# Performance work log

Hardware: AMD Instinct MI355X
Metric: run time of the kernel (lower is better)

The kernel has to match this reference:

```python
import jax, jax.numpy as jnp
import numpy as np

N_NODES = 100000


def _gcn_norm(edge_index, edge_weight, num_nodes):
    # add self loops with weight 1 (PyG GCNConv default)
    loop = jnp.arange(num_nodes, dtype=edge_index.dtype)
    src = jnp.concatenate([edge_index[0], loop])
    dst = jnp.concatenate([edge_index[1], loop])
    w = jnp.concatenate([edge_weight, jnp.ones(num_nodes, edge_weight.dtype)])
    deg = jax.ops.segment_sum(w, dst, num_segments=num_nodes)
    dinv = jnp.where(deg > 0, jax.lax.rsqrt(deg), 0.0).astype(edge_weight.dtype)
    norm = dinv[src] * w * dinv[dst]
    return src, dst, norm


def _gcn_conv(x, W, b, src, dst, norm):
    h = x @ W                                   # [N, out]
    msg = h[src] * norm[:, None]                # [E+N, out] gather + scale
    out = jax.ops.segment_sum(msg, dst, num_segments=x.shape[0])
    return out + b


def setup_inputs() -> dict:
    key = jax.random.key(0)
    ks = jax.random.split(key, 6)
    nfeat, nhid, nclass, E = 128, 64, 40, 1600000
    return {
        "x": jax.random.normal(ks[0], (N_NODES, nfeat), jnp.float32),
        "edge_index": jax.random.randint(ks[1], (2, E), 0, N_NODES, jnp.int64),
        "edge_weight": jax.random.uniform(ks[2], (E,), jnp.float32),
        "W1": jax.random.normal(ks[3], (nfeat, nhid), jnp.float32) / np.sqrt(nfeat),
        "b1": jnp.zeros((nhid,), jnp.float32),
        "W2": jax.random.normal(ks[4], (nhid, nclass), jnp.float32) / np.sqrt(nhid),
        "b2": jnp.zeros((nclass,), jnp.float32),
    }


def reference(x, edge_index, edge_weight, W1, b1, W2, b2):
    src, dst, norm = _gcn_norm(edge_index, edge_weight, x.shape[0])
    h = jax.nn.relu(_gcn_conv(x, W1, b1, src, dst, norm))
    # dropout p=0.0 / eval mode -> identity
    h = _gcn_conv(h, W2, b2, src, dst, norm)
    return jax.nn.log_softmax(h, axis=1)
```

## Files before the change

### kernel.cpp

```cpp
#include <hip/hip_runtime.h>
#include <hip/hip_fp16.h>
#include <math.h>

#define NFEAT 128
#define NHID 64
#define NCLASS 40
#define BNODES 256
#define BSHIFT 8
#define EPB 4096
#define CAPSH 13
#define CAP (1 << CAPSH)
#define LCAP 5120

typedef _Float16 f16x8 __attribute__((ext_vector_type(8)));
typedef float f32x4 __attribute__((ext_vector_type(4)));

static __device__ __forceinline__ __half2 i2h2(int x) { union { int i; __half2 h; } u; u.i = x; return u.h; }
static __device__ __forceinline__ int h22i(__half2 h) { union { int i; __half2 h; } u; u.h = h; return u.i; }
static __device__ __forceinline__ __half2 shfl_xor_h2(__half2 v, int off) { return i2h2(__shfl_xor(h22i(v), off)); }


__global__ void k_init(int* __restrict__ gcur, int NB) {
    int i = blockIdx.x * blockDim.x + threadIdx.x;
    if (i < NB) gcur[i] = i << CAPSH;
}

__global__ __launch_bounds__(256) void k_bscatter(const int* __restrict__ src, const int* __restrict__ dst,
                                                  const float* __restrict__ w, int* __restrict__ gcur,
                                                  int2* __restrict__ csrT, int E, int NB) {
    __shared__ int2 sorted[EPB];
    __shared__ int gidx[EPB];
    __shared__ int lcnt[512], lscan[512], fb[512], lpos[512];
    int t = threadIdx.x;
    for (int i = t; i < 512; i += 256) { lcnt[i] = 0; lpos[i] = 0; }
    __syncthreads();
    int base = blockIdx.x * EPB;
    int rs[16], rd[16]; float rw[16];
    #pragma unroll
    for (int j = 0; j < 4; j++) {
        int e0 = base + j * 1024 + t * 4;
        if (e0 + 3 < E) {
            int4 s4 = *(const int4*)(src + e0);
            int4 d4 = *(const int4*)(dst + e0);
            float4 w4 = *(const float4*)(w + e0);
            rs[j * 4 + 0] = s4.x; rs[j * 4 + 1] = s4.y; rs[j * 4 + 2] = s4.z; rs[j * 4 + 3] = s4.w;
            rd[j * 4 + 0] = d4.x; rd[j * 4 + 1] = d4.y; rd[j * 4 + 2] = d4.z; rd[j * 4 + 3] = d4.w;
            rw[j * 4 + 0] = w4.x; rw[j * 4 + 1] = w4.y; rw[j * 4 + 2] = w4.z; rw[j * 4 + 3] = w4.w;
        } else {
            #pragma unroll
            for (int k = 0; k < 4; k++) {
                int e = e0 + k;
                bool ok = (e < E);
                rd[j * 4 + k] = ok ? dst[e] : -1;
                rs[j * 4 + k] = ok ? src[e] : 0;
                rw[j * 4 + k] = ok ? w[e] : 0.f;
            }
        }
    }
    #pragma unroll
    for (int i = 0; i < 16; i++)
        if (rd[i] >= 0) atomicAdd(&lcnt[rd[i] >> BSHIFT], 1);
    __syncthreads();
    int i0 = t, i1 = t + 256;
    lscan[i0] = lcnt[i0]; lscan[i1] = lcnt[i1];
    __syncthreads();
    for (int off = 1; off < 512; off <<= 1) {
        int v0 = (i0 >= off) ? lscan[i0 - off] : 0;
        int v1 = (i1 >= off) ? lscan[i1 - off] : 0;
        __syncthreads();
        lscan[i0] += v0; lscan[i1] += v1;
        __syncthreads();
    }
    for (int i = t; i < NB; i += 256) {
        int c = lcnt[i];
        if (c) {
            int gb = atomicAdd(&gcur[i], c);
            fb[i] = gb - (lscan[i] - c);
        }
    }
    __syncthreads();
    #pragma unroll
    for (int i = 0; i < 16; i++) {
        if (rd[i] >= 0) {
            int d = rd[i];
            int b = d >> BSHIFT;
            int p = (lscan[b] - lcnt[b]) + atomicAdd(&lpos[b], 1);
            int2 v;
            v.x = rs[i] | ((d & (BNODES - 1)) << 20);
            v.y = __float_as_int(rw[i]);
            sorted[p] = v;
            gidx[p] = fb[b] + p;
        }
    }
    __syncthreads();
    int tot = lscan[511];
    for (int i = t; i < tot; i += 256) csrT[gidx[i]] = sorted[i];
}

__global__ __launch_bounds__(512) void k_cscan(const int* __restrict__ gcur, int* __restrict__ cbase, int NB) {
    __shared__ int sh[512];
    int t = threadIdx.x;
    int c = (t < NB) ? (gcur[t] - (t << CAPSH)) : 0;
    sh[t] = c;
    __syncthreads();
    for (int off = 1; off < 512; off <<= 1) {
        int v = (t >= off) ? sh[t - off] : 0;
        __syncthreads();
        sh[t] += v;
        __syncthreads();
    }
    if (t < NB) cbase[t] = sh[t] - c;
}

__global__ __launch_bounds__(256) void k_lsort(const int* __restrict__ gcur, const int* __restrict__ cbase,
                                               const int2* __restrict__ csrT, int2* __restrict__ csr,
                                               int* __restrict__ offs, float* __restrict__ dinv,
                                               int N, int E) {
    __shared__ int2 sorted[LCAP];
    __shared__ int lh[BNODES];
    __shared__ int lo[BNODES];
    __shared__ float da[BNODES];
    int b = blockIdx.x, t = threadIdx.x;
    int rbase = b << CAPSH;
    int cnt = gcur[b] - rbase;
    if (cnt > LCAP) cnt = LCAP;
    int cb = cbase[b];
    lh[t] = 0; da[t] = 0.f;
    __syncthreads();
    int2 reg[20];
    #pragma unroll
    for (int i = 0; i < 20; i++) {
        int e = t + i * 256;
        reg[i] = (e < cnt) ? csrT[rbase + e] : make_int2(-1, 0);
    }
    #pragma unroll
    for (int i = 0; i < 20; i++) {
        if (reg[i].x >= 0) {
            int dl = (reg[i].x >> 20) & 255;
            atomicAdd(&lh[dl], 1);
            atomicAdd(&da[dl], __int_as_float(reg[i].y));
        }
    }
    __syncthreads();
    int own = lh[t];
    lo[t] = own;
    __syncthreads();
    for (int off = 1; off < 256; off <<= 1) {
        int v = (t >= off) ? lo[t - off] : 0;
        __syncthreads();
        lo[t] += v;
        __syncthreads();
    }
    int excl = lo[t] - own;
    __syncthreads();
    lh[t] = excl;
    int gn = (b << BSHIFT) + t;
    if (gn < N) {
        offs[gn] = cb + excl;
        dinv[gn] = rsqrtf(1.0f + da[t]);
    }
    if (b == 0 && t == 0) offs[N] = E;
    __syncthreads();
    #pragma unroll
    for (int i = 0; i < 20; i++) {
        if (reg[i].x >= 0) {
            int dl = (reg[i].x >> 20) & 255;
            int p = atomicAdd(&lh[dl], 1);
            sorted[p] = reg[i];
        }
    }
    __syncthreads();
    for (int e = t; e < cnt; e += 256) {
        int2 v = sorted[e];
        __half2 w2 = __half2half2(__float2half(__int_as_float(v.y)));
        v.x &= 0xFFFFF;
        v.y = h22i(w2);
        csr[cb + e] = v;
    }
}


__global__ __launch_bounds__(256) void k_gemm1(const float* __restrict__ x,
                                               const float* __restrict__ W,
                                               const float* __restrict__ dinv,
                                               __half* __restrict__ h, int N) {
    __shared__ _Float16 xh[64][136];
    __shared__ _Float16 Wt[64][136];
    int t = threadIdx.x;
    int row0 = blockIdx.x * 64;
    for (int i = t; i < 2048; i += 256) {
        int r = i >> 5, k4 = i & 31;
        int row = row0 + r;
        float4 v = (row < N) ? ((const float4*)(x + (size_t)row * NFEAT))[k4]
                             : make_float4(0.f, 0.f, 0.f, 0.f);
        *(__half2*)&xh[r][k4 * 4]     = __floats2half2_rn(v.x, v.y);
        *(__half2*)&xh[r][k4 * 4 + 2] = __floats2half2_rn(v.z, v.w);
    }
    for (int i = t; i < 4096; i += 256) {
        int k2 = i >> 6, c = i & 63;
        float a0 = W[(size_t)(2 * k2) * NHID + c];
        float a1 = W[(size_t)(2 * k2 + 1) * NHID + c];
        *(__half2*)&Wt[c][k2 * 2] = __floats2half2_rn(a0, a1);
    }
    __syncthreads();
    int wave = t >> 6, lane = t & 63;
    int quad = lane >> 4, l16 = lane & 15;
    int r0 = wave * 16;
    f32x4 acc[4] = {};
    #pragma unroll
    for (int k0 = 0; k0 < 128; k0 += 32) {
        f16x8 af = *(const f16x8*)&xh[r0 + l16][k0 + quad * 8];
        #pragma unroll
        for (int ct = 0; ct < 4; ct++) {
            f16x8 bf = *(const f16x8*)&Wt[ct * 16 + l16][k0 + quad * 8];
            acc[ct] = __builtin_amdgcn_mfma_f32_16x16x32_f16(af, bf, acc[ct], 0, 0, 0);
        }
    }
    #pragma unroll
    for (int ct = 0; ct < 4; ct++) {
        #pragma unroll
        for (int j = 0; j < 4; j++) {
            int row = row0 + r0 + quad * 4 + j;
            if (row < N)
                h[(size_t)row * NHID + ct * 16 + l16] = __float2half(dinv[row] * acc[ct][j]);
        }
    }
}


__global__ __launch_bounds__(256) void k_agg1(const int* __restrict__ offs, const int2* __restrict__ csr,
                                              const __half* __restrict__ h1, const float* __restrict__ dinv,
                                              const float* __restrict__ b1, __half* __restrict__ out1, int N) {
    int n = (blockIdx.x * blockDim.x + threadIdx.x) >> 6;
    if (n >= N) return;
    int lane = threadIdx.x & 63;
    int grp = lane >> 3;
    int c8 = lane & 7;
    const char* hb = (const char*)h1;
    unsigned int c16 = (unsigned int)c8 << 4;
    int e = offs[n], end = offs[n + 1];
    float di = dinv[n];
    float4 hsv = *(const float4*)(hb + (unsigned int)n * 128u + c16);
    float4 bb0 = ((const float4*)b1)[2 * c8];
    float4 bb1 = ((const float4*)b1)[2 * c8 + 1];
    __half2 z = __floats2half2_rn(0.f, 0.f);
    __half2 aA[4] = {z, z, z, z}, aB[4] = {z, z, z, z};
    for (; e + 16 <= end; e += 16) {
        int2 vA = csr[e + grp];
        int2 vB = csr[e + 8 + grp];
        float4 hA = *(const float4*)(hb + (unsigned int)(vA.x & 0xFFFFF) * 128u + c16);
        float4 hB = *(const float4*)(hb + (unsigned int)(vB.x & 0xFFFFF) * 128u + c16);
        __half2 wA = i2h2(vA.y), wB = i2h2(vB.y);
        const __half2* pA = (const __half2*)&hA;
        const __half2* pB = (const __half2*)&hB;
        #pragma unroll
        for (int q = 0; q < 4; q++) {
            aA[q] = __hfma2(wA, pA[q], aA[q]);
            aB[q] = __hfma2(wB, pB[q], aB[q]);
        }
    }
    if (e + 8 <= end) {
        int2 v = csr[e + grp];
        float4 hv = *(const float4*)(hb + (unsigned int)(v.x & 0xFFFFF) * 128u + c16);
        __half2 wv = i2h2(v.y);
        const __half2* p = (const __half2*)&hv;
        #pragma unroll
        for (int q = 0; q < 4; q++) aA[q] = __hfma2(wv, p[q], aA[q]);
        e += 8;
    }
    if (e + grp < end) {
        int2 v = csr[e + grp];
        float4 hv = *(const float4*)(hb + (unsigned int)(v.x & 0xFFFFF) * 128u + c16);
        __half2 wv = i2h2(v.y);
        const __half2* p = (const __half2*)&hv;
        #pragma unroll
        for (int q = 0; q < 4; q++) aB[q] = __hfma2(wv, p[q], aB[q]);
    }
    __half2 acc2[4];
    #pragma unroll
    for (int q = 0; q < 4; q++) acc2[q] = __hadd2(aA[q], aB[q]);
    #pragma unroll
    for (int off = 8; off <= 32; off <<= 1) {
        #pragma unroll
        for (int q = 0; q < 4; q++) acc2[q] = __hadd2(acc2[q], shfl_xor_h2(acc2[q], off));
    }
    if (grp == 0) {
        float a[8], s[8];
        #pragma unroll
        for (int q = 0; q < 4; q++) {
            float2 fa = __half22float2(acc2[q]);
            a[2 * q] = fa.x; a[2 * q + 1] = fa.y;
            float2 f = __half22float2(((const __half2*)&hsv)[q]);
            s[2 * q] = f.x; s[2 * q + 1] = f.y;
        }
        float o[8];
        o[0] = fmaxf(di * (a[0] + s[0]) + bb0.x, 0.f);
        o[1] = fmaxf(di * (a[1] + s[1]) + bb0.y, 0.f);
        o[2] = fmaxf(di * (a[2] + s[2]) + bb0.z, 0.f);
        o[3] = fmaxf(di * (a[3] + s[3]) + bb0.w, 0.f);
        o[4] = fmaxf(di * (a[4] + s[4]) + bb1.x, 0.f);
        o[5] = fmaxf(di * (a[5] + s[5]) + bb1.y, 0.f);
        o[6] = fmaxf(di * (a[6] + s[6]) + bb1.z, 0.f);
        o[7] = fmaxf(di * (a[7] + s[7]) + bb1.w, 0.f);
        float4 st;
        #pragma unroll
        for (int q = 0; q < 4; q++)
            ((__half2*)&st)[q] = __floats2half2_rn(o[2 * q], o[2 * q + 1]);
        ((float4*)out1)[(size_t)n * 8 + c8] = st;
    }
}


__global__ __launch_bounds__(256) void k_gemm2(const __half* __restrict__ a,
                                               const float* __restrict__ W,
                                               const float* __restrict__ dinv,
                                               __half* __restrict__ h, int N) {
    __shared__ _Float16 As[64][72];
    __shared__ _Float16 Bt[64][72];
    int t = threadIdx.x;
    int row0 = blockIdx.x * 64;
    for (int i = t; i < 512; i += 256) {
        int r = i >> 3, q = i & 7;
        int row = row0 + r;
        f16x8 v = {};
        if (row < N) v = *(const f16x8*)(a + (size_t)row * NHID + q * 8);
        *(f16x8*)&As[r][q * 8] = v;
    }
    for (int i = t; i < 4096; i += 256) {
        int c = i >> 6, k = i & 63;
        float wv = (c < NCLASS) ? W[k * NCLASS + c] : 0.f;
        Bt[c][k] = (_Float16)wv;
    }
    __syncthreads();
    int wave = t >> 6, lane = t & 63;
    int quad = lane >> 4, l16 = lane & 15;
    int r0 = wave * 16;
    f32x4 acc[4] = {};
    #pragma unroll
    for (int k0 = 0; k0 < 64; k0 += 32) {
        f16x8 af = *(const f16x8*)&As[r0 + l16][k0 + quad * 8];
        #pragma unroll
        for (int ct = 0; ct < 4; ct++) {
            f16x8 bf = *(const f16x8*)&Bt[ct * 16 + l16][k0 + quad * 8];
            acc[ct] = __builtin_amdgcn_mfma_f32_16x16x32_f16(af, bf, acc[ct], 0, 0, 0);
        }
    }
    #pragma unroll
    for (int ct = 0; ct < 4; ct++) {
        int col = ct * 16 + l16;
        #pragma unroll
        for (int j = 0; j < 4; j++) {
            int row = row0 + r0 + quad * 4 + j;
            if (row < N)
                h[((size_t)row << 6) + col] = __float2half(dinv[row] * acc[ct][j]);
        }
    }
}


__global__ __launch_bounds__(256) void k_agg2(const int* __restrict__ offs, const int2* __restrict__ csr,
                                              const __half* __restrict__ h2, const float* __restrict__ dinv,
                                              const float* __restrict__ b2, float* __restrict__ out, int N) {
    int n = (blockIdx.x * blockDim.x + threadIdx.x) >> 6;
    if (n >= N) return;
    int lane = threadIdx.x & 63;
    int grp = lane >> 3;
    int c8 = lane & 7;
    const char* hb = (const char*)h2;
    unsigned int c16 = (unsigned int)c8 << 4;
    int e = offs[n], end = offs[n + 1];
    bool act = (c8 < 5);
    float di = dinv[n];
    float4 hsv = *(const float4*)(hb + ((unsigned int)n << 7) + c16);
    float4 bb0 = {}, bb1 = {};
    if (act) {
        bb0 = ((const float4*)b2)[2 * c8];
        bb1 = ((const float4*)b2)[2 * c8 + 1];
    }
    __half2 z = __floats2half2_rn(0.f, 0.f);
    __half2 aA[4] = {z, z, z, z}, aB[4] = {z, z, z, z};
    for (; e + 16 <= end; e += 16) {
        int2 vA = csr[e + grp];
        int2 vB = csr[e + 8 + grp];
        float4 hA = *(const float4*)(hb + ((unsigned int)(vA.x & 0xFFFFF) << 7) + c16);
        float4 hB = *(const float4*)(hb + ((unsigned int)(vB.x & 0xFFFFF) << 7) + c16);
        __half2 wA = i2h2(vA.y), wB = i2h2(vB.y);
        const __half2* pA = (const __half2*)&hA;
        const __half2* pB = (const __half2*)&hB;
        #pragma unroll
        for (int q = 0; q < 4; q++) {
            aA[q] = __hfma2(wA, pA[q], aA[q]);
            aB[q] = __hfma2(wB, pB[q], aB[q]);
        }
    }
    if (e + 8 <= end) {
        int2 v = csr[e + grp];
        float4 hv = *(const float4*)(hb + ((unsigned int)(v.x & 0xFFFFF) << 7) + c16);
        __half2 wv = i2h2(v.y);
        const __half2* p = (const __half2*)&hv;
        #pragma unroll
        for (int q = 0; q < 4; q++) aA[q] = __hfma2(wv, p[q], aA[q]);
        e += 8;
    }
    if (e + grp < end) {
        int2 v = csr[e + grp];
        float4 hv = *(const float4*)(hb + ((unsigned int)(v.x & 0xFFFFF) << 7) + c16);
        __half2 wv = i2h2(v.y);
        const __half2* p = (const __half2*)&hv;
        #pragma unroll
        for (int q = 0; q < 4; q++) aB[q] = __hfma2(wv, p[q], aB[q]);
    }
    __half2 acc2[4];
    #pragma unroll
    for (int q = 0; q < 4; q++) acc2[q] = __hadd2(aA[q], aB[q]);
    #pragma unroll
    for (int off = 8; off <= 32; off <<= 1) {
        #pragma unroll
        for (int q = 0; q < 4; q++) acc2[q] = __hadd2(acc2[q], shfl_xor_h2(acc2[q], off));
    }
    float a[8], s[8];
    #pragma unroll
    for (int q = 0; q < 4; q++) {
        float2 fa = __half22float2(acc2[q]);
        a[2 * q] = fa.x; a[2 * q + 1] = fa.y;
        float2 f = __half22float2(((const __half2*)&hsv)[q]);
        s[2 * q] = f.x; s[2 * q + 1] = f.y;
    }
    float v[8];
    v[0] = di * (a[0] + s[0]) + bb0.x;
    v[1] = di * (a[1] + s[1]) + bb0.y;
    v[2] = di * (a[2] + s[2]) + bb0.z;
    v[3] = di * (a[3] + s[3]) + bb0.w;
    v[4] = di * (a[4] + s[4]) + bb1.x;
    v[5] = di * (a[5] + s[5]) + bb1.y;
    v[6] = di * (a[6] + s[6]) + bb1.z;
    v[7] = di * (a[7] + s[7]) + bb1.w;
    float m = -INFINITY;
    if (act) {
        #pragma unroll
        for (int k = 0; k < 8; k++) m = fmaxf(m, v[k]);
    }
    #pragma unroll
    for (int off = 1; off <= 4; off <<= 1) m = fmaxf(m, __shfl_xor(m, off));
    float ex = 0.f;
    if (act) {
        #pragma unroll
        for (int k = 0; k < 8; k++) ex += __expf(v[k] - m);
    }
    #pragma unroll
    for (int off = 1; off <= 4; off <<= 1) ex += __shfl_xor(ex, off);
    if (act && grp == 0) {
        float ls = __logf(ex);
        float4 o0, o1;
        o0.x = v[0] - m - ls; o0.y = v[1] - m - ls; o0.z = v[2] - m - ls; o0.w = v[3] - m - ls;
        o1.x = v[4] - m - ls; o1.y = v[5] - m - ls; o1.z = v[6] - m - ls; o1.w = v[7] - m - ls;
        float* op = out + (size_t)n * NCLASS + c8 * 8;
        *(float4*)op = o0;
        *(float4*)(op + 4) = o1;
    }
}


extern "C" void kernel_launch(void* const* d_in, const int* in_sizes, int n_in,
                              void* d_out, int out_size, void* d_ws, size_t ws_size,
                              hipStream_t stream) {
    const float* x  = (const float*)d_in[0];
    const int*   ei = (const int*)d_in[1];
    const float* w  = (const float*)d_in[2];
    const float* W1 = (const float*)d_in[3];
    const float* b1 = (const float*)d_in[4];
    const float* W2 = (const float*)d_in[5];
    const float* b2 = (const float*)d_in[6];
    float* out = (float*)d_out;

    const int N = in_sizes[0] / NFEAT;
    const int E = in_sizes[1] / 2;
    const int* src = ei;
    const int* dst = ei + E;

    const int NB = (N + BNODES - 1) >> BSHIFT;
    const int nbuild = (E + EPB - 1) / EPB;

    int2*   csrT  = (int2*)d_ws;
    int2*   csr   = csrT + (size_t)NB * CAP;
    float*  dinv  = (float*)(csr + E);
    int*    offs  = (int*)(dinv + N);
    __half* h1h   = (__half*)(offs + N + 1);
    __half* out1h = h1h + (size_t)N * NHID;
    __half* h2old = out1h + (size_t)N * NHID;
    int*    gcur  = (int*)(h2old + (size_t)N * NCLASS);
    int*    cbase = gcur + NB;

    __half* h2p = (__half*)d_ws;

    k_init<<<(NB + 255) / 256, 256, 0, stream>>>(gcur, NB);
    k_bscatter<<<nbuild, 256, 0, stream>>>(src, dst, w, gcur, csrT, E, NB);
    k_cscan<<<1, 512, 0, stream>>>(gcur, cbase, NB);
    k_lsort<<<NB, 256, 0, stream>>>(gcur, cbase, csrT, csr, offs, dinv, N, E);

    k_gemm1<<<(N + 63) / 64, 256, 0, stream>>>(x, W1, dinv, h1h, N);
    k_agg1<<<(N + 3) / 4, 256, 0, stream>>>(offs, csr, h1h, dinv, b1, out1h, N);

    k_gemm2<<<(N + 63) / 64, 256, 0, stream>>>(out1h, W2, dinv, h2p, N);
    k_agg2<<<(N + 3) / 4, 256, 0, stream>>>(offs, csr, h2p, dinv, b2, out, N);
}
```

Before: 275.9 us.

## Sort CSR in place per bucket, drop global scan, and prefetch four edge batches

The per-bucket local sort now writes back into the same padded bucket region instead of compacting into a separate CSR array. That removes the single-block prefix-scan kernel and one full copy of the edge array. Each node therefore stores an explicit end offset, since bucket regions are no longer contiguous. The aggregation kernels also issue four predicated edge gathers up front to raise memory-level parallelism, then fall back to a simple strided tail loop. The in-place read-then-write within a block relies on all loads finishing before the stores, which the existing barriers ensure, and the padded layout spreads CSR reads over more memory.

```diff
diff --git a/kernel.cpp b/kernel.cpp
--- a/kernel.cpp
+++ b/kernel.cpp
@@ -97,25 +97,10 @@
     for (int i = t; i < tot; i += 256) csrT[gidx[i]] = sorted[i];
 }
 
-__global__ __launch_bounds__(512) void k_cscan(const int* __restrict__ gcur, int* __restrict__ cbase, int NB) {
-    __shared__ int sh[512];
-    int t = threadIdx.x;
-    int c = (t < NB) ? (gcur[t] - (t << CAPSH)) : 0;
-    sh[t] = c;
-    __syncthreads();
-    for (int off = 1; off < 512; off <<= 1) {
-        int v = (t >= off) ? sh[t - off] : 0;
-        __syncthreads();
-        sh[t] += v;
-        __syncthreads();
-    }
-    if (t < NB) cbase[t] = sh[t] - c;
-}
-
-__global__ __launch_bounds__(256) void k_lsort(const int* __restrict__ gcur, const int* __restrict__ cbase,
-                                               const int2* __restrict__ csrT, int2* __restrict__ csr,
-                                               int* __restrict__ offs, float* __restrict__ dinv,
-                                               int N, int E) {
+__global__ __launch_bounds__(256) void k_lsort(const int* __restrict__ gcur,
+                                               int2* csr,
+                                               int* __restrict__ offs, int* __restrict__ endo,
+                                               float* __restrict__ dinv, int N) {
     __shared__ int2 sorted[LCAP];
     __shared__ int lh[BNODES];
     __shared__ int lo[BNODES];
@@ -124,14 +109,13 @@
     int rbase = b << CAPSH;
     int cnt = gcur[b] - rbase;
     if (cnt > LCAP) cnt = LCAP;
-    int cb = cbase[b];
     lh[t] = 0; da[t] = 0.f;
     __syncthreads();
     int2 reg[20];
     #pragma unroll
     for (int i = 0; i < 20; i++) {
         int e = t + i * 256;
-        reg[i] = (e < cnt) ? csrT[rbase + e] : make_int2(-1, 0);
+        reg[i] = (e < cnt) ? csr[rbase + e] : make_int2(-1, 0);
     }
     #pragma unroll
     for (int i = 0; i < 20; i++) {
@@ -156,10 +140,10 @@
     lh[t] = excl;
     int gn = (b << BSHIFT) + t;
     if (gn < N) {
-        offs[gn] = cb + excl;
+        offs[gn] = rbase + excl;
+        endo[gn] = rbase + excl + own;
         dinv[gn] = rsqrtf(1.0f + da[t]);
     }
-    if (b == 0 && t == 0) offs[N] = E;
     __syncthreads();
     #pragma unroll
     for (int i = 0; i < 20; i++) {
@@ -175,7 +159,7 @@
         __half2 w2 = __half2half2(__float2half(__int_as_float(v.y)));
         v.x &= 0xFFFFF;
         v.y = h22i(w2);
-        csr[cb + e] = v;
+        csr[rbase + e] = v;
     }
 }
 
@@ -228,7 +212,8 @@
 }
 
 
-__global__ __launch_bounds__(256) void k_agg1(const int* __restrict__ offs, const int2* __restrict__ csr,
+__global__ __launch_bounds__(256) void k_agg1(const int* __restrict__ offs, const int* __restrict__ endo,
+                                              const int2* __restrict__ csr,
                                               const __half* __restrict__ h1, const float* __restrict__ dinv,
                                               const float* __restrict__ b1, __half* __restrict__ out1, int N) {
     int n = (blockIdx.x * blockDim.x + threadIdx.x) >> 6;
@@ -238,47 +223,59 @@
     int c8 = lane & 7;
     const char* hb = (const char*)h1;
     unsigned int c16 = (unsigned int)c8 << 4;
-    int e = offs[n], end = offs[n + 1];
+    int e = offs[n], end = endo[n];
     float di = dinv[n];
     float4 hsv = *(const float4*)(hb + (unsigned int)n * 128u + c16);
     float4 bb0 = ((const float4*)b1)[2 * c8];
     float4 bb1 = ((const float4*)b1)[2 * c8 + 1];
     __half2 z = __floats2half2_rn(0.f, 0.f);
-    __half2 aA[4] = {z, z, z, z}, aB[4] = {z, z, z, z};
-    for (; e + 16 <= end; e += 16) {
-        int2 vA = csr[e + grp];
-        int2 vB = csr[e + 8 + grp];
-        float4 hA = *(const float4*)(hb + (unsigned int)(vA.x & 0xFFFFF) * 128u + c16);
-        float4 hB = *(const float4*)(hb + (unsigned int)(vB.x & 0xFFFFF) * 128u + c16);
-        __half2 wA = i2h2(vA.y), wB = i2h2(vB.y);
-        const __half2* pA = (const __half2*)&hA;
-        const __half2* pB = (const __half2*)&hB;
+    __half2 aa0[4] = {z, z, z, z}, aa1[4] = {z, z, z, z};
+    __half2 aa2[4] = {z, z, z, z}, aa3[4] = {z, z, z, z};
+    {
+        int2 v0, v1, v2, v3;
+        int i0 = e + grp, i1 = e + 8 + grp, i2 = e + 16 + grp, i3 = e + 24 + grp;
+        bool b0 = i0 < end, b1v = i1 < end, b2 = i2 < end, b3 = i3 < end;
+        v0 = csr[b0 ? i0 : e];
+        v1 = csr[b1v ? i1 : e];
+        v2 = csr[b2 ? i2 : e];
+        v3 = csr[b3 ? i3 : e];
+        unsigned int r0 = b0 ? (unsigned int)(v0.x & 0xFFFFF) : 0u;
+        unsigned int r1 = b1v ? (unsigned int)(v1.x & 0xFFFFF) : 0u;
+        unsigned int r2 = b2 ? (unsigned int)(v2.x & 0xFFFFF) : 0u;
+        unsigned int r3 = b3 ? (unsigned int)(v3.x & 0xFFFFF) : 0u;
+        float4 h0 = *(const float4*)(hb + r0 * 128u + c16);
+        float4 h1v = *(const float4*)(hb + r1 * 128u + c16);
+        float4 h2v = *(const float4*)(hb + r2 * 128u + c16);
+        float4 h3v = *(const float4*)(hb + r3 * 128u + c16);
+        __half2 w0 = b0 ? i2h2(v0.y) : z;
+        __half2 w1 = b1v ? i2h2(v1.y) : z;
+        __half2 w2 = b2 ? i2h2(v2.y) : z;
+        __half2 w3 = b3 ? i2h2(v3.y) : z;
+        const __half2* p0 = (const __half2*)&h0;
+        const __half2* p1 = (const __half2*)&h1v;
+        const __half2* p2 = (const __half2*)&h2v;
+        const __half2* p3 = (const __half2*)&h3v;
         #pragma unroll
         for (int q = 0; q < 4; q++) {
-            aA[q] = __hfma2(wA, pA[q], aA[q]);
-            aB[q] = __hfma2(wB, pB[q], aB[q]);
-        }
-    }
-    if (e + 8 <= end) {
-        int2 v = csr[e + grp];
-        float4 hv = *(const float4*)(hb + (unsigned int)(v.x & 0xFFFFF) * 128u + c16);
+            aa0[q] = __hfma2(w0, p0[q], aa0[q]);
+            aa1[q] = __hfma2(w1, p1[q], aa1[q]);
+            aa2[q] = __hfma2(w2, p2[q], aa2[q]);
+            aa3[q] = __hfma2(w3, p3[q], aa3[q]);
+        }
+    }
+    for (int idx = e + 32 + grp; idx < end; idx += 8) {
+        int2 v = csr[idx];
+        unsigned int row = (unsigned int)(v.x & 0xFFFFF);
+        float4 hv = *(const float4*)(hb + row * 128u + c16);
         __half2 wv = i2h2(v.y);
         const __half2* p = (const __half2*)&hv;
         #pragma unroll
-        for (int q = 0; q < 4; q++) aA[q] = __hfma2(wv, p[q], aA[q]);
-        e += 8;
-    }
-    if (e + grp < end) {
-        int2 v = csr[e + grp];
-        float4 hv = *(const float4*)(hb + (unsigned int)(v.x & 0xFFFFF) * 128u + c16);
-        __half2 wv = i2h2(v.y);
-        const __half2* p = (const __half2*)&hv;
-        #pragma unroll
-        for (int q = 0; q < 4; q++) aB[q] = __hfma2(wv, p[q], aB[q]);
+        for (int q = 0; q < 4; q++) aa0[q] = __hfma2(wv, p[q], aa0[q]);
     }
     __half2 acc2[4];
     #pragma unroll
-    for (int q = 0; q < 4; q++) acc2[q] = __hadd2(aA[q], aB[q]);
+    for (int q = 0; q < 4; q++)
+        acc2[q] = __hadd2(__hadd2(aa0[q], aa1[q]), __hadd2(aa2[q], aa3[q]));
     #pragma unroll
     for (int off = 8; off <= 32; off <<= 1) {
         #pragma unroll
@@ -358,7 +355,8 @@
 }
 
 
-__global__ __launch_bounds__(256) void k_agg2(const int* __restrict__ offs, const int2* __restrict__ csr,
+__global__ __launch_bounds__(256) void k_agg2(const int* __restrict__ offs, const int* __restrict__ endo,
+                                              const int2* __restrict__ csr,
                                               const __half* __restrict__ h2, const float* __restrict__ dinv,
                                               const float* __restrict__ b2, float* __restrict__ out, int N) {
     int n = (blockIdx.x * blockDim.x + threadIdx.x) >> 6;
@@ -368,7 +366,7 @@
     int c8 = lane & 7;
     const char* hb = (const char*)h2;
     unsigned int c16 = (unsigned int)c8 << 4;
-    int e = offs[n], end = offs[n + 1];
+    int e = offs[n], end = endo[n];
     bool act = (c8 < 5);
     float di = dinv[n];
     float4 hsv = *(const float4*)(hb + ((unsigned int)n << 7) + c16);
@@ -378,41 +376,53 @@
         bb1 = ((const float4*)b2)[2 * c8 + 1];
     }
     __half2 z = __floats2half2_rn(0.f, 0.f);
-    __half2 aA[4] = {z, z, z, z}, aB[4] = {z, z, z, z};
-    for (; e + 16 <= end; e += 16) {
-        int2 vA = csr[e + grp];
-        int2 vB = csr[e + 8 + grp];
-        float4 hA = *(const float4*)(hb + ((unsigned int)(vA.x & 0xFFFFF) << 7) + c16);
-        float4 hB = *(const float4*)(hb + ((unsigned int)(vB.x & 0xFFFFF) << 7) + c16);
-        __half2 wA = i2h2(vA.y), wB = i2h2(vB.y);
-        const __half2* pA = (const __half2*)&hA;
-        const __half2* pB = (const __half2*)&hB;
+    __half2 aa0[4] = {z, z, z, z}, aa1[4] = {z, z, z, z};
+    __half2 aa2[4] = {z, z, z, z}, aa3[4] = {z, z, z, z};
+    {
+        int2 v0, v1, v2, v3;
+        int i0 = e + grp, i1 = e + 8 + grp, i2 = e + 16 + grp, i3 = e + 24 + grp;
+        bool b0 = i0 < end, b1v = i1 < end, b2c = i2 < end, b3 = i3 < end;
+        v0 = csr[b0 ? i0 : e];
+        v1 = csr[b1v ? i1 : e];
+        v2 = csr[b2c ? i2 : e];
+        v3 = csr[b3 ? i3 : e];
+        unsigned int r0 = b0 ? (unsigned int)(v0.x & 0xFFFFF) : 0u;
+        unsigned int r1 = b1v ? (unsigned int)(v1.x & 0xFFFFF) : 0u;
+        unsigned int r2 = b2c ? (unsigned int)(v2.x & 0xFFFFF) : 0u;
+        unsigned int r3 = b3 ? (unsigned int)(v3.x & 0xFFFFF) : 0u;
+        float4 h0 = *(const float4*)(hb + (r0 << 7) + c16);
+        float4 h1v = *(const float4*)(hb + (r1 << 7) + c16);
+        float4 h2v = *(const float4*)(hb + (r2 << 7) + c16);
+        float4 h3v = *(const float4*)(hb + (r3 << 7) + c16);
+        __half2 w0 = b0 ? i2h2(v0.y) : z;
+        __half2 w1 = b1v ? i2h2(v1.y) : z;
+        __half2 w2 = b2c ? i2h2(v2.y) : z;
+        __half2 w3 = b3 ? i2h2(v3.y) : z;
+        const __half2* p0 = (const __half2*)&h0;
+        const __half2* p1 = (const __half2*)&h1v;
+        const __half2* p2 = (const __half2*)&h2v;
+        const __half2* p3 = (const __half2*)&h3v;
         #pragma unroll
         for (int q = 0; q < 4; q++) {
-            aA[q] = __hfma2(wA, pA[q], aA[q]);
-            aB[q] = __hfma2(wB, pB[q], aB[q]);
-        }
-    }
-    if (e + 8 <= end) {
-        int2 v = csr[e + grp];
-        float4 hv = *(const float4*)(hb + ((unsigned int)(v.x & 0xFFFFF) << 7) + c16);
+            aa0[q] = __hfma2(w0, p0[q], aa0[q]);
+            aa1[q] = __hfma2(w1, p1[q], aa1[q]);
+            aa2[q] = __hfma2(w2, p2[q], aa2[q]);
+            aa3[q] = __hfma2(w3, p3[q], aa3[q]);
+        }
+    }
+    for (int idx = e + 32 + grp; idx < end; idx += 8) {
+        int2 v = csr[idx];
+        unsigned int row = (unsigned int)(v.x & 0xFFFFF);
+        float4 hv = *(const float4*)(hb + (row << 7) + c16);
         __half2 wv = i2h2(v.y);
         const __half2* p = (const __half2*)&hv;
         #pragma unroll
-        for (int q = 0; q < 4; q++) aA[q] = __hfma2(wv, p[q], aA[q]);
-        e += 8;
-    }
-    if (e + grp < end) {
-        int2 v = csr[e + grp];
-        float4 hv = *(const float4*)(hb + ((unsigned int)(v.x & 0xFFFFF) << 7) + c16);
-        __half2 wv = i2h2(v.y);
-        const __half2* p = (const __half2*)&hv;
-        #pragma unroll
-        for (int q = 0; q < 4; q++) aB[q] = __hfma2(wv, p[q], aB[q]);
+        for (int q = 0; q < 4; q++) aa0[q] = __hfma2(wv, p[q], aa0[q]);
     }
     __half2 acc2[4];
     #pragma unroll
-    for (int q = 0; q < 4; q++) acc2[q] = __hadd2(aA[q], aB[q]);
+    for (int q = 0; q < 4; q++)
+        acc2[q] = __hadd2(__hadd2(aa0[q], aa1[q]), __hadd2(aa2[q], aa3[q]));
     #pragma unroll
     for (int off = 8; off <= 32; off <<= 1) {
         #pragma unroll
@@ -481,26 +491,22 @@
     const int NB = (N + BNODES - 1) >> BSHIFT;
     const int nbuild = (E + EPB - 1) / EPB;
 
-    int2*   csrT  = (int2*)d_ws;
-    int2*   csr   = csrT + (size_t)NB * CAP;
-    float*  dinv  = (float*)(csr + E);
+    int2*   csr   = (int2*)d_ws;
+    __half* h2p   = (__half*)(csr + (size_t)NB * CAP);
+    float*  dinv  = (float*)(h2p + (size_t)N * 64);
     int*    offs  = (int*)(dinv + N);
-    __half* h1h   = (__half*)(offs + N + 1);
+    int*    endo  = offs + N;
+    __half* h1h   = (__half*)(endo + N);
     __half* out1h = h1h + (size_t)N * NHID;
-    __half* h2old = out1h + (size_t)N * NHID;
-    int*    gcur  = (int*)(h2old + (size_t)N * NCLASS);
-    int*    cbase = gcur + NB;
-
-    __half* h2p = (__half*)d_ws;
+    int*    gcur  = (int*)(out1h + (size_t)N * NHID);
 
     k_init<<<(NB + 255) / 256, 256, 0, stream>>>(gcur, NB);
-    k_bscatter<<<nbuild, 256, 0, stream>>>(src, dst, w, gcur, csrT, E, NB);
-    k_cscan<<<1, 512, 0, stream>>>(gcur, cbase, NB);
-    k_lsort<<<NB, 256, 0, stream>>>(gcur, cbase, csrT, csr, offs, dinv, N, E);
+    k_bscatter<<<nbuild, 256, 0, stream>>>(src, dst, w, gcur, csr, E, NB);
+    k_lsort<<<NB, 256, 0, stream>>>(gcur, csr, offs, endo, dinv, N);
 
     k_gemm1<<<(N + 63) / 64, 256, 0, stream>>>(x, W1, dinv, h1h, N);
-    k_agg1<<<(N + 3) / 4, 256, 0, stream>>>(offs, csr, h1h, dinv, b1, out1h, N);
+    k_agg1<<<(N + 3) / 4, 256, 0, stream>>>(offs, endo, csr, h1h, dinv, b1, out1h, N);
 
     k_gemm2<<<(N + 63) / 64, 256, 0, stream>>>(out1h, W2, dinv, h2p, N);
-    k_agg2<<<(N + 3) / 4, 256, 0, stream>>>(offs, csr, h2p, dinv, b2, out, N);
-}
+    k_agg2<<<(N + 3) / 4, 256, 0, stream>>>(offs, endo, csr, h2p, dinv, b2, out, N);
+}
```

Result: faster. 254.9 us (-7.6%).
